# Optimization experiments

Hardware: AMD Instinct MI355X
Metric: run time of the kernel (lower is better)

## Reference

```python
import jax, jax.numpy as jnp
import numpy as np
from jax import lax

V, E, NL, NS, DC, EX = 32000, 1024, 4, 16, 4, 2
DI = EX * E          # 2048 inner dim
DTR = E // 16        # 64 dt_rank
BSZ, L = 2, 512
EPS = 1e-5


def setup_inputs() -> dict:
    key = jax.random.key(0)
    ks = jax.random.split(key, 12)
    s = 0.02
    emb = jax.random.normal(ks[0], (V, E), jnp.float32) * s
    ln_w = jnp.ones((NL, E), jnp.float32)
    ln_b = jnp.zeros((NL, E), jnp.float32)
    in_proj_w = jax.random.normal(ks[1], (NL, 2 * DI, E), jnp.float32) * s
    conv_w = jax.random.normal(ks[2], (NL, DI, DC), jnp.float32) * 0.1
    conv_b = jnp.zeros((NL, DI), jnp.float32)
    x_proj_w = jax.random.normal(ks[3], (NL, DTR + 2 * NS, DI), jnp.float32) * s
    dt_proj_w = jax.random.normal(ks[4], (NL, DI, DTR), jnp.float32) * s
    dt_proj_b = jax.random.normal(ks[5], (NL, DI), jnp.float32) * 0.1
    # canonical S4D-real init: A[d,n] = n+1  ->  A_log = log(A)
    A_log = jnp.log(jnp.tile(jnp.arange(1, NS + 1, dtype=jnp.float32)[None, None, :], (NL, DI, 1)))
    D_param = jnp.ones((NL, DI), jnp.float32)
    out_proj_w = jax.random.normal(ks[6], (NL, E, DI), jnp.float32) * s
    fln_w = jnp.ones((E,), jnp.float32)
    fln_b = jnp.zeros((E,), jnp.float32)
    input_ids = jax.random.randint(ks[7], (BSZ, L), 0, V, jnp.int64)
    targets = jax.random.randint(ks[8], (BSZ, L), 0, V, jnp.int64)
    return dict(input_ids=input_ids, targets=targets, emb=emb, ln_w=ln_w, ln_b=ln_b,
                in_proj_w=in_proj_w, conv_w=conv_w, conv_b=conv_b, x_proj_w=x_proj_w,
                dt_proj_w=dt_proj_w, dt_proj_b=dt_proj_b, A_log=A_log, D_param=D_param,
                out_proj_w=out_proj_w, fln_w=fln_w, fln_b=fln_b)


def _layer_norm(x, w, b):
    mu = x.mean(-1, keepdims=True)
    var = ((x - mu) ** 2).mean(-1, keepdims=True)
    return (x - mu) * lax.rsqrt(var + EPS) * w + b


def _mamba_block(x, in_w, cw, cb, xw, dtw, dtb, a_log, d_par, ow):
    # x: (B,L,E)
    xz = jnp.einsum('ble,fe->blf', x, in_w)          # (B,L,2*DI)
    u, res = jnp.split(xz, 2, axis=-1)               # each (B,L,DI)
    # causal depthwise conv1d, kernel width DC (left pad DC-1)
    u_pad = jnp.pad(u, ((0, 0), (DC - 1, 0), (0, 0)))
    u_conv = sum(cw[:, k] * u_pad[:, k:k + u.shape[1], :] for k in range(DC))
    u = jax.nn.silu(u_conv + cb)
    x_dbl = jnp.einsum('bld,fd->blf', u, xw)         # (B,L,DTR+2*NS)
    dt = x_dbl[..., :DTR]
    Bm = x_dbl[..., DTR:DTR + NS]                    # (B,L,NS)
    Cm = x_dbl[..., DTR + NS:]                       # (B,L,NS)
    delta = jax.nn.softplus(jnp.einsum('blr,dr->bld', dt, dtw) + dtb)  # (B,L,DI)
    A = -jnp.exp(a_log)                              # (DI,NS)
    dA = jnp.exp(delta[..., None] * A)               # (B,L,DI,NS)
    dBu = delta[..., None] * Bm[:, :, None, :] * u[..., None]

    def step(h, inp):
        dA_t, dBu_t, C_t = inp
        h = dA_t * h + dBu_t                         # (B,DI,NS)
        y = jnp.einsum('bdn,bn->bd', h, C_t)
        return h, y

    h0 = jnp.zeros((x.shape[0], DI, NS), x.dtype)
    _, ys = lax.scan(step, h0, (dA.transpose(1, 0, 2, 3), dBu.transpose(1, 0, 2, 3), Cm.transpose(1, 0, 2)))
    y = ys.transpose(1, 0, 2) + u * d_par            # (B,L,DI)
    y = y * jax.nn.silu(res)
    return jnp.einsum('bld,ed->ble', y, ow)


def reference(input_ids, targets, emb, ln_w, ln_b, in_proj_w, conv_w, conv_b,
              x_proj_w, dt_proj_w, dt_proj_b, A_log, D_param, out_proj_w, fln_w, fln_b):
    x = emb[input_ids]                               # (B,L,E)
    for l in range(NL):
        h = _layer_norm(x, ln_w[l], ln_b[l])
        h = _mamba_block(h, in_proj_w[l], conv_w[l], conv_b[l], x_proj_w[l],
                         dt_proj_w[l], dt_proj_b[l], A_log[l], D_param[l], out_proj_w[l])
        x = x + h
    x = _layer_norm(x, fln_w, fln_b)
    logits = jnp.einsum('ble,ve->blv', x, emb)       # tied lm_head
    logp = jax.nn.log_softmax(logits, axis=-1)
    valid = targets != -1
    safe_t = jnp.where(valid, targets, 0)
    nll = -jnp.take_along_axis(logp, safe_t[..., None], axis=-1)[..., 0]
    loss = jnp.where(valid, nll, 0.0).mean()
    return logits, loss
```

## Files before the change

### kernel.cpp

```cpp
#include <hip/hip_runtime.h>
#include <cstdint>
#include <cstddef>

#define L_SEQ 512
#define NBATCH 2
#define NTOK 1024
#define E_DIM 1024
#define V_DIM 32000
#define DI_DIM 2048
#define NS_DIM 16
#define DTR_DIM 64
#define DC_DIM 4
#define NL_DIM 4
#define NC 8
#define LC (L_SEQ / NC)

typedef __bf16 bf16;
typedef __bf16 bf16x8 __attribute__((ext_vector_type(8)));
typedef __bf16 bf16x4 __attribute__((ext_vector_type(4)));
typedef float  f32x4  __attribute__((ext_vector_type(4)));

__device__ __forceinline__ void gload_lds16(const void* g, void* l)
{
    __builtin_amdgcn_global_load_lds((const __attribute__((address_space(1))) uint32_t*)g,
                                     (__attribute__((address_space(3))) uint32_t*)l, 16, 0, 0);
}

__device__ __forceinline__ float softplusf(float z)
{
    return fmaxf(z, 0.0f) + log1pf(expf(-fabsf(z)));
}

__global__ void cast_f32_to_bf16(const float* __restrict__ in, bf16* __restrict__ out, int n4)
{
    int stride = gridDim.x * blockDim.x;
    for (int i = blockIdx.x * blockDim.x + threadIdx.x; i < n4; i += stride) {
        f32x4 v = ((const f32x4*)in)[i];
        bf16x4 o;
        o[0] = (bf16)v[0]; o[1] = (bf16)v[1]; o[2] = (bf16)v[2]; o[3] = (bf16)v[3];
        ((bf16x4*)out)[i] = o;
    }
}

__global__ void cast3_kernel(const float* __restrict__ a, bf16* __restrict__ oa, int na4,
                             const float* __restrict__ b, bf16* __restrict__ ob, int nb4,
                             const float* __restrict__ c, bf16* __restrict__ oc, int nc4)
{
    int stride = gridDim.x * blockDim.x;
    int tot = na4 + nb4 + nc4;
    for (int i = blockIdx.x * blockDim.x + threadIdx.x; i < tot; i += stride) {
        const float* src; bf16* dst; int k = i;
        if (k < na4) { src = a; dst = oa; }
        else if ((k -= na4) < nb4) { src = b; dst = ob; }
        else { k -= nb4; src = c; dst = oc; }
        f32x4 v = ((const f32x4*)src)[k];
        bf16x4 o;
        o[0] = (bf16)v[0]; o[1] = (bf16)v[1]; o[2] = (bf16)v[2]; o[3] = (bf16)v[3];
        ((bf16x4*)dst)[k] = o;
    }
}

__global__ void embed_kernel(const int* __restrict__ ids, const float* __restrict__ emb,
                             float* __restrict__ x)
{
    int t = blockIdx.x;
    int id = ids[t];
    ((f32x4*)(x + (size_t)t * E_DIM))[threadIdx.x] =
        ((const f32x4*)(emb + (size_t)id * E_DIM))[threadIdx.x];
}

__global__ void ln_kernel(const float* __restrict__ x, const float* __restrict__ w,
                          const float* __restrict__ b, bf16* __restrict__ out)
{
    int t = blockIdx.x;
    int tid = threadIdx.x;
    f32x4 v = ((const f32x4*)(x + (size_t)t * E_DIM))[tid];
    float s  = v[0] + v[1] + v[2] + v[3];
    float sq = v[0]*v[0] + v[1]*v[1] + v[2]*v[2] + v[3]*v[3];
#pragma unroll
    for (int off = 1; off < 64; off <<= 1) { s += __shfl_xor(s, off); sq += __shfl_xor(sq, off); }
    __shared__ float ps[4], pq[4];
    if ((tid & 63) == 0) { ps[tid >> 6] = s; pq[tid >> 6] = sq; }
    __syncthreads();
    float S  = ps[0] + ps[1] + ps[2] + ps[3];
    float SQ = pq[0] + pq[1] + pq[2] + pq[3];
    float mu  = S * (1.0f / E_DIM);
    float var = SQ * (1.0f / E_DIM) - mu * mu;
    float rs  = rsqrtf(var + 1e-5f);
    f32x4 wv = ((const f32x4*)w)[tid];
    f32x4 bv = ((const f32x4*)b)[tid];
    bf16x4 o;
#pragma unroll
    for (int i = 0; i < 4; ++i) o[i] = (bf16)((v[i] - mu) * rs * wv[i] + bv[i]);
    ((bf16x4*)(out + (size_t)t * E_DIM))[tid] = o;
}

template<int BM, int BN, int MODE, int SK>
__global__ __launch_bounds__(256) void gemm_bt(const bf16* __restrict__ A, const bf16* __restrict__ B,
                                               void* __restrict__ Cv, int K,
                                               int lda, int ldb, int ldc,
                                               const float* __restrict__ bias,
                                               int RB, int CB, int CBpad)
{
    int pid = blockIdx.x;
    int per = RB * CBpad;
    int sk  = pid / per;
    int rem = pid - sk * per;
    int xcd = rem & 7;
    int j   = rem >> 3;
    int cpx = CBpad >> 3;
    int rb  = j % RB;
    int cb  = xcd * cpx + j / RB;
    if (cb >= CB) return;
    int kseg = K / SK;
    int kbeg = sk * kseg;
    int kend = kbeg + kseg;

    __shared__ __align__(16) bf16 As[BM * 32];
    __shared__ __align__(16) bf16 Bs[BN * 32];
    int tid  = threadIdx.x;
    int lane = tid & 63;
    int wid  = tid >> 6;
    int wr = wid >> 1, wc = wid & 1;
    int li = lane & 15, lg = lane >> 4;
    const bf16* Ablk = A + (size_t)(rb * BM) * lda;
    const bf16* Bblk = B + (size_t)(cb * BN) * ldb;
    constexpr int MR  = BM / 32;
    constexpr int NR  = BN / 32;
    constexpr int TOT = (BM + BN) * 4;
    f32x4 acc[MR][NR] = {};
    for (int k0 = kbeg; k0 < kend; k0 += 32) {
        __syncthreads();
#pragma unroll
        for (int it = 0; it < TOT / 256; ++it) {
            int wbase = it * 256 + wid * 64;
            int idx   = wbase + lane;
            if (wbase < BM * 4) {
                int row = idx >> 2, seg = idx & 3;
                gload_lds16(Ablk + (size_t)row * lda + k0 + seg * 8, As + (size_t)wbase * 8);
            } else {
                int bb  = wbase - BM * 4;
                int bi  = bb + lane;
                int row = bi >> 2, seg = bi & 3;
                gload_lds16(Bblk + (size_t)row * ldb + k0 + seg * 8, Bs + (size_t)bb * 8);
            }
        }
        __syncthreads();
        bf16x8 af[MR], bfr[NR];
#pragma unroll
        for (int m = 0; m < MR; ++m) af[m]  = *(const bf16x8*)&As[(wr * (BM/2) + m * 16 + li) * 32 + lg * 8];
#pragma unroll
        for (int n = 0; n < NR; ++n) bfr[n] = *(const bf16x8*)&Bs[(wc * (BN/2) + n * 16 + li) * 32 + lg * 8];
#pragma unroll
        for (int m = 0; m < MR; ++m)
#pragma unroll
            for (int n = 0; n < NR; ++n)
                acc[m][n] = __builtin_amdgcn_mfma_f32_16x16x32_bf16(af[m], bfr[n], acc[m][n], 0, 0, 0);
    }
    int row0 = rb * BM + wr * (BM/2);
    int col0 = cb * BN + wc * (BN/2);
    float* Cf = (float*)Cv;
    bf16*  Cb = (bf16*)Cv;
#pragma unroll
    for (int m = 0; m < MR; ++m) {
#pragma unroll
        for (int n = 0; n < NR; ++n) {
            int r = row0 + m * 16 + lg * 4;
            int c = col0 + n * 16 + li;
#pragma unroll
            for (int q = 0; q < 4; ++q) {
                float v = acc[m][n][q];
                if (MODE == 0) {
                    Cf[(size_t)(r + q) * ldc + c] = v;
                } else if (MODE == 1) {
                    float* cp = Cf + (size_t)(r + q) * ldc + c;
                    *cp = v + *cp;
                } else if (MODE == 2) {
                    Cb[(size_t)(r + q) * ldc + c] = (bf16)softplusf(v + bias[c]);
                } else if (MODE == 4) {
                    Cb[(size_t)(r + q) * ldc + c] = (bf16)v;
                } else if (MODE == 5) {
                    atomicAdd(Cf + (size_t)(r + q) * ldc + c, v);
                }
            }
        }
    }
}

template<int BM, int BN, int MODE, int SK = 1>
static void launch_gemm(const bf16* A, const bf16* B, void* C, int M, int N, int K,
                        int lda, int ldb, int ldc, const float* bias, hipStream_t stream)
{
    int RB = M / BM;
    int CB = (N + BN - 1) / BN;
    int CBpad = (CB + 7) & ~7;
    gemm_bt<BM, BN, MODE, SK><<<RB * CBpad * SK, 256, 0, stream>>>(A, B, C, K, lda, ldb, ldc,
                                                                   bias, RB, CB, CBpad);
}

__global__ __launch_bounds__(256) void cxk_kernel(
        const bf16* __restrict__ xz, const float* __restrict__ cw,
        const float* __restrict__ cb, const float* __restrict__ xw,
        float* __restrict__ xdbl, bf16* __restrict__ dt_bf, bf16* __restrict__ u_bf)
{
    int t0  = blockIdx.x * 4;
    int bb  = t0 >> 9;
    int tid = threadIdx.x;
    int f   = tid & 127;
    int ks  = tid >> 7;
    __shared__ __align__(16) float sxz[7][256];
    __shared__ __align__(16) float su[4][256];
    __shared__ float pacc[4][128];
    float acc[4] = {0, 0, 0, 0};
    for (int kc = 0; kc < DI_DIM; kc += 256) {
        __syncthreads();
        if (tid < 224) {
            int row = tid >> 5, c8 = (tid & 31) * 8;
            int tr = t0 - 3 + row;
            float vals[8] = {0, 0, 0, 0, 0, 0, 0, 0};
            if (tr >= bb * L_SEQ) {
                bf16x8 v = *(const bf16x8*)&xz[(size_t)tr * (2 * DI_DIM) + kc + c8];
#pragma unroll
                for (int jj = 0; jj < 8; ++jj) vals[jj] = (float)v[jj];
            }
#pragma unroll
            for (int jj = 0; jj < 8; ++jj) sxz[row][c8 + jj] = vals[jj];
        }
        __syncthreads();
        {
            int c = tid;
            const float* cwp = cw + (size_t)(kc + c) * DC_DIM;
            float w0 = cwp[0], w1 = cwp[1], w2 = cwp[2], w3 = cwp[3];
            float bs = cb[kc + c];
#pragma unroll
            for (int tt = 0; tt < 4; ++tt) {
                float a = bs + w0 * sxz[tt][c] + w1 * sxz[tt + 1][c]
                             + w2 * sxz[tt + 2][c] + w3 * sxz[tt + 3][c];
                float uo = a / (1.0f + __expf(-a));
                su[tt][c] = uo;
                u_bf[(size_t)(t0 + tt) * DI_DIM + kc + c] = (bf16)uo;
            }
        }
        __syncthreads();
        if (f < 96) {
            int kb = ks * 128;
            for (int kk = kb; kk < kb + 128; kk += 4) {
                f32x4 wv = *(const f32x4*)&xw[(size_t)f * DI_DIM + kc + kk];
#pragma unroll
                for (int tt = 0; tt < 4; ++tt) {
                    f32x4 uv = *(f32x4*)&su[tt][kk];
                    acc[tt] += wv[0]*uv[0] + wv[1]*uv[1] + wv[2]*uv[2] + wv[3]*uv[3];
                }
            }
        }
    }
    if (ks == 1 && f < 96) {
#pragma unroll
        for (int tt = 0; tt < 4; ++tt) pacc[tt][f] = acc[tt];
    }
    __syncthreads();
    if (ks == 0 && f < 96) {
#pragma unroll
        for (int tt = 0; tt < 4; ++tt) {
            float v = acc[tt] + pacc[tt][f];
            xdbl[(size_t)(t0 + tt) * 96 + f] = v;
            if (f < 64) dt_bf[(size_t)(t0 + tt) * DTR_DIM + f] = (bf16)v;
        }
    }
}

__global__ __launch_bounds__(256) void scan_phase_a(
        const bf16* __restrict__ delta, const float* __restrict__ xdbl,
        const bf16* __restrict__ u_bf, const float* __restrict__ A_log,
        float* __restrict__ Pbuf, float* __restrict__ Sbuf)
{
    int tid = threadIdx.x;
    int c   = blockIdx.x & (NC - 1);
    int dblk= (blockIdx.x >> 3) & 127;
    int b   = blockIdx.x >> 10;
    int d0  = dblk << 4;
    int n = tid & 15, dl = tid >> 4;
    int d = d0 + dl;
    float Ac = -expf(A_log[(size_t)d * NS_DIM + n]);
    float h = 0.0f, P = 1.0f;
    __shared__ float s_dlt[32][16], s_u[32][16], s_B[32][16];
    int tt0 = tid >> 4, cc = tid & 15;
    int tbase = b * L_SEQ + c * LC;
    for (int t0 = 0; t0 < LC; t0 += 32) {
        __syncthreads();
#pragma unroll
        for (int jj = 0; jj < 2; ++jj) {
            int tt = jj * 16 + tt0;
            size_t trow = (size_t)(tbase + t0 + tt);
            s_dlt[tt][cc] = (float)delta[trow * DI_DIM + d0 + cc];
            s_u[tt][cc]   = (float)u_bf[trow * DI_DIM + d0 + cc];
            s_B[tt][cc]   = xdbl[trow * 96 + 64 + cc];
        }
        __syncthreads();
#pragma unroll
        for (int t = 0; t < 32; ++t) {
            float dlt = s_dlt[t][dl];
            float dA  = __expf(dlt * Ac);
            h = fmaf(dA, h, dlt * s_B[t][n] * s_u[t][dl]);
            P *= dA;
        }
    }
    size_t oi = (((size_t)(b * NC + c) * DI_DIM) + d) * NS_DIM + n;
    Pbuf[oi] = P;
    Sbuf[oi] = h;
}

__global__ __launch_bounds__(256) void scan_phase_c(
        const bf16* __restrict__ delta, const float* __restrict__ xdbl,
        const bf16* __restrict__ u_bf, const bf16* __restrict__ xz,
        const float* __restrict__ A_log, const float* __restrict__ D_par,
        const float* __restrict__ Pbuf, const float* __restrict__ Sbuf,
        bf16* __restrict__ y)
{
    int tid = threadIdx.x;
    int c   = blockIdx.x & (NC - 1);
    int dblk= (blockIdx.x >> 3) & 127;
    int b   = blockIdx.x >> 10;
    int d0  = dblk << 4;
    int n = tid & 15, dl = tid >> 4;
    int d = d0 + dl;
    float Ac = -expf(A_log[(size_t)d * NS_DIM + n]);
    float Dp = D_par[d];
    float h = 0.0f;
    for (int cp = 0; cp < c; ++cp) {
        size_t oi = (((size_t)(b * NC + cp) * DI_DIM) + d) * NS_DIM + n;
        h = fmaf(Pbuf[oi], h, Sbuf[oi]);
    }
    __shared__ float s_dlt[32][16], s_u[32][16], s_res[32][16], s_B[32][16], s_C[32][16];
    __shared__ bf16  s_y[32][16];
    int tt0 = tid >> 4, cc = tid & 15;
    int tbase = b * L_SEQ + c * LC;
    for (int t0 = 0; t0 < LC; t0 += 32) {
        __syncthreads();
#pragma unroll
        for (int jj = 0; jj < 2; ++jj) {
            int tt = jj * 16 + tt0;
            size_t trow = (size_t)(tbase + t0 + tt);
            s_dlt[tt][cc] = (float)delta[trow * DI_DIM + d0 + cc];
            s_u[tt][cc]   = (float)u_bf[trow * DI_DIM + d0 + cc];
            s_res[tt][cc] = (float)xz[trow * (2 * DI_DIM) + DI_DIM + d0 + cc];
            s_B[tt][cc]   = xdbl[trow * 96 + 64 + cc];
            s_C[tt][cc]   = xdbl[trow * 96 + 80 + cc];
        }
        __syncthreads();
#pragma unroll
        for (int t = 0; t < 32; ++t) {
            float dlt = s_dlt[t][dl];
            float uu  = s_u[t][dl];
            float dA  = __expf(dlt * Ac);
            float dBu = dlt * s_B[t][n] * uu;
            h = fmaf(dA, h, dBu);
            float yp = h * s_C[t][n];
            yp += __shfl_xor(yp, 1);
            yp += __shfl_xor(yp, 2);
            yp += __shfl_xor(yp, 4);
            yp += __shfl_xor(yp, 8);
            if (n == 0) {
                float res = s_res[t][dl];
                float yv  = fmaf(uu, Dp, yp) * (res / (1.0f + __expf(-res)));
                s_y[t][dl] = (bf16)yv;
            }
        }
        __syncthreads();
#pragma unroll
        for (int jj = 0; jj < 2; ++jj) {
            int tt = jj * 16 + tt0;
            size_t trow = (size_t)(tbase + t0 + tt);
            y[trow * DI_DIM + d0 + cc] = s_y[tt][cc];
        }
    }
}

__global__ void lse_nll_kernel(const float* __restrict__ logits, const int* __restrict__ targets,
                               float* __restrict__ lossp)
{
    int t = blockIdx.x, tid = threadIdx.x;
    const f32x4* row = (const f32x4*)(logits + (size_t)t * V_DIM);
    float m = -1e30f, s = 0.0f;
    for (int i = tid; i < V_DIM / 4; i += 256) {
        f32x4 v = row[i];
        float m4 = fmaxf(fmaxf(v[0], v[1]), fmaxf(v[2], v[3]));
        if (m4 > m) { s *= __expf(m - m4); m = m4; }
        s += __expf(v[0] - m) + __expf(v[1] - m) + __expf(v[2] - m) + __expf(v[3] - m);
    }
#pragma unroll
    for (int off = 1; off < 64; off <<= 1) {
        float mo = __shfl_xor(m, off), so = __shfl_xor(s, off);
        float nm = fmaxf(m, mo);
        s = s * __expf(m - nm) + so * __expf(mo - nm);
        m = nm;
    }
    __shared__ float pm[4], ps2[4];
    if ((tid & 63) == 0) { pm[tid >> 6] = m; ps2[tid >> 6] = s; }
    __syncthreads();
    if (tid == 0) {
        float M = fmaxf(fmaxf(pm[0], pm[1]), fmaxf(pm[2], pm[3]));
        float S = ps2[0] * __expf(pm[0] - M) + ps2[1] * __expf(pm[1] - M)
                + ps2[2] * __expf(pm[2] - M) + ps2[3] * __expf(pm[3] - M);
        int tg = targets[t];
        if (tg >= 0) {
            float v = (M + logf(S)) - logits[(size_t)t * V_DIM + tg];
            atomicAdd(lossp, v * (1.0f / NTOK));
        }
    }
}

extern "C" void kernel_launch(void* const* d_in, const int* in_sizes, int n_in,
                              void* d_out, int out_size, void* d_ws, size_t ws_size,
                              hipStream_t stream)
{
    const int*   ids   = (const int*)d_in[0];
    const int*   tgt   = (const int*)d_in[1];
    const float* emb   = (const float*)d_in[2];
    const float* ln_w  = (const float*)d_in[3];
    const float* ln_b  = (const float*)d_in[4];
    const float* inw   = (const float*)d_in[5];
    const float* convw = (const float*)d_in[6];
    const float* convb = (const float*)d_in[7];
    const float* xw    = (const float*)d_in[8];
    const float* dtw   = (const float*)d_in[9];
    const float* dtb   = (const float*)d_in[10];
    const float* alog  = (const float*)d_in[11];
    const float* dpar  = (const float*)d_in[12];
    const float* outw  = (const float*)d_in[13];
    const float* flnw  = (const float*)d_in[14];
    const float* flnb  = (const float*)d_in[15];
    float* logits = (float*)d_out;
    float* lossp  = logits + (size_t)NTOK * V_DIM;

    char* wsp = (char*)d_ws;
    size_t off = 0;
    auto alloc = [&](size_t bytes) -> void* {
        void* p = wsp + off;
        off += (bytes + 255) & ~(size_t)255;
        return p;
    };
    bf16*  emb_bf  = (bf16*)alloc((size_t)V_DIM * E_DIM * 2);
    bf16*  winl    = (bf16*)alloc((size_t)2 * DI_DIM * E_DIM * 2);
    bf16*  woutl   = (bf16*)alloc((size_t)E_DIM * DI_DIM * 2);
    bf16*  wdtl    = (bf16*)alloc((size_t)DI_DIM * DTR_DIM * 2);
    float* x       = (float*)alloc((size_t)NTOK * E_DIM * 4);
    bf16*  h_bf    = (bf16*)alloc((size_t)NTOK * E_DIM * 2);
    bf16*  xzb     = (bf16*)alloc((size_t)NTOK * 2 * DI_DIM * 2);
    bf16*  u_bf    = (bf16*)alloc((size_t)NTOK * DI_DIM * 2);
    float* xdbl    = (float*)alloc((size_t)NTOK * 96 * 4);
    bf16*  dt_bf   = (bf16*)alloc((size_t)NTOK * DTR_DIM * 2);
    bf16*  deltab  = (bf16*)alloc((size_t)NTOK * DI_DIM * 2);
    bf16*  y_bf    = (bf16*)alloc((size_t)NTOK * DI_DIM * 2);
    bf16*  xf_bf   = (bf16*)alloc((size_t)NTOK * E_DIM * 2);
    float* Pbuf    = (float*)alloc((size_t)NBATCH * NC * DI_DIM * NS_DIM * 4);
    float* Sbuf    = (float*)alloc((size_t)NBATCH * NC * DI_DIM * NS_DIM * 4);
    if (off > ws_size) return;

    hipMemsetAsync(lossp, 0, sizeof(float), stream);
    {
        int n4 = (int)((size_t)V_DIM * E_DIM / 4);
        cast_f32_to_bf16<<<4096, 256, 0, stream>>>(emb, emb_bf, n4);
    }
    embed_kernel<<<NTOK, 256, 0, stream>>>(ids, emb, x);

    for (int l = 0; l < NL_DIM; ++l) {
        cast3_kernel<<<2048, 256, 0, stream>>>(
            inw  + (size_t)l * 2 * DI_DIM * E_DIM, winl,  (int)((size_t)2 * DI_DIM * E_DIM / 4),
            outw + (size_t)l * E_DIM * DI_DIM,     woutl, (int)((size_t)E_DIM * DI_DIM / 4),
            dtw  + (size_t)l * DI_DIM * DTR_DIM,   wdtl,  (int)((size_t)DI_DIM * DTR_DIM / 4));

        ln_kernel<<<NTOK, 256, 0, stream>>>(x, ln_w + l * E_DIM, ln_b + l * E_DIM, h_bf);
        launch_gemm<128, 64, 4>(h_bf, winl, xzb, NTOK, 2 * DI_DIM, E_DIM,
                                E_DIM, E_DIM, 2 * DI_DIM, nullptr, stream);
        cxk_kernel<<<NTOK / 4, 256, 0, stream>>>(
            xzb, convw + (size_t)l * DI_DIM * DC_DIM, convb + (size_t)l * DI_DIM,
            xw + (size_t)l * 96 * DI_DIM, xdbl, dt_bf, u_bf);
        launch_gemm<64, 64, 2>(dt_bf, wdtl, deltab, NTOK, DI_DIM, DTR_DIM,
                               DTR_DIM, DTR_DIM, DI_DIM, dtb + (size_t)l * DI_DIM, stream);
        scan_phase_a<<<NBATCH * (DI_DIM / 16) * NC, 256, 0, stream>>>(
            deltab, xdbl, u_bf, alog + (size_t)l * DI_DIM * NS_DIM, Pbuf, Sbuf);
        scan_phase_c<<<NBATCH * (DI_DIM / 16) * NC, 256, 0, stream>>>(
            deltab, xdbl, u_bf, xzb, alog + (size_t)l * DI_DIM * NS_DIM,
            dpar + (size_t)l * DI_DIM, Pbuf, Sbuf, y_bf);
        launch_gemm<128, 128, 5, 4>(y_bf, woutl, x, NTOK, E_DIM, DI_DIM,
                                    DI_DIM, DI_DIM, E_DIM, nullptr, stream);
    }
    ln_kernel<<<NTOK, 256, 0, stream>>>(x, flnw, flnb, xf_bf);
    launch_gemm<128, 128, 0>(xf_bf, emb_bf, logits, NTOK, V_DIM, E_DIM,
                             E_DIM, E_DIM, V_DIM, nullptr, stream);
    lse_nll_kernel<<<NTOK, 256, 0, stream>>>(logits, tgt, lossp);
}
```

Baseline: 852.4 us.

## Fuse dt_proj into conv kernel, batch weight casts, and use BK=64 GEMM tiles

The dt_proj GEMM plus softplus is folded into the conv/x_proj kernel as a scalar FMA loop over dt_proj weights held in fp32, which removes one launch and the dt_bf round trip. Weight casts for all layers now run in one kernel up front when the workspace is large enough, replacing four per-layer casts. The GEMM template gains a BK parameter and all GEMMs now use K tiles of 64, halving barrier count per K step at the cost of more LDS. The fused dt loop reads 2048x64 fp32 weights per block, which could add redundant global traffic.

```diff
diff --git a/kernel.cpp b/kernel.cpp
--- a/kernel.cpp
+++ b/kernel.cpp
@@ -42,17 +42,15 @@
     }
 }
 
-__global__ void cast3_kernel(const float* __restrict__ a, bf16* __restrict__ oa, int na4,
-                             const float* __restrict__ b, bf16* __restrict__ ob, int nb4,
-                             const float* __restrict__ c, bf16* __restrict__ oc, int nc4)
+__global__ void cast2_kernel(const float* __restrict__ a, bf16* __restrict__ oa, int na4,
+                             const float* __restrict__ b, bf16* __restrict__ ob, int nb4)
 {
     int stride = gridDim.x * blockDim.x;
-    int tot = na4 + nb4 + nc4;
+    int tot = na4 + nb4;
     for (int i = blockIdx.x * blockDim.x + threadIdx.x; i < tot; i += stride) {
         const float* src; bf16* dst; int k = i;
         if (k < na4) { src = a; dst = oa; }
-        else if ((k -= na4) < nb4) { src = b; dst = ob; }
-        else { k -= nb4; src = c; dst = oc; }
+        else { k -= na4; src = b; dst = ob; }
         f32x4 v = ((const f32x4*)src)[k];
         bf16x4 o;
         o[0] = (bf16)v[0]; o[1] = (bf16)v[1]; o[2] = (bf16)v[2]; o[3] = (bf16)v[3];
@@ -95,11 +93,10 @@
     ((bf16x4*)(out + (size_t)t * E_DIM))[tid] = o;
 }
 
-template<int BM, int BN, int MODE, int SK>
+template<int BM, int BN, int BK, int MODE, int SK>
 __global__ __launch_bounds__(256) void gemm_bt(const bf16* __restrict__ A, const bf16* __restrict__ B,
                                                void* __restrict__ Cv, int K,
                                                int lda, int ldb, int ldc,
-                                               const float* __restrict__ bias,
                                                int RB, int CB, int CBpad)
 {
     int pid = blockIdx.x;
@@ -116,8 +113,8 @@
     int kbeg = sk * kseg;
     int kend = kbeg + kseg;
 
-    __shared__ __align__(16) bf16 As[BM * 32];
-    __shared__ __align__(16) bf16 Bs[BN * 32];
+    __shared__ __align__(16) bf16 As[BM * BK];
+    __shared__ __align__(16) bf16 Bs[BN * BK];
     int tid  = threadIdx.x;
     int lane = tid & 63;
     int wid  = tid >> 6;
@@ -125,37 +122,44 @@
     int li = lane & 15, lg = lane >> 4;
     const bf16* Ablk = A + (size_t)(rb * BM) * lda;
     const bf16* Bblk = B + (size_t)(cb * BN) * ldb;
-    constexpr int MR  = BM / 32;
-    constexpr int NR  = BN / 32;
-    constexpr int TOT = (BM + BN) * 4;
+    constexpr int MR   = BM / 32;
+    constexpr int NR   = BN / 32;
+    constexpr int SEGS = BK / 8;
+    constexpr int AOPS = BM * SEGS;
+    constexpr int TOT  = (BM + BN) * SEGS;
     f32x4 acc[MR][NR] = {};
-    for (int k0 = kbeg; k0 < kend; k0 += 32) {
+    for (int k0 = kbeg; k0 < kend; k0 += BK) {
         __syncthreads();
 #pragma unroll
         for (int it = 0; it < TOT / 256; ++it) {
             int wbase = it * 256 + wid * 64;
             int idx   = wbase + lane;
-            if (wbase < BM * 4) {
-                int row = idx >> 2, seg = idx & 3;
+            if (wbase < AOPS) {
+                int row = idx / SEGS, seg = idx % SEGS;
                 gload_lds16(Ablk + (size_t)row * lda + k0 + seg * 8, As + (size_t)wbase * 8);
             } else {
-                int bb  = wbase - BM * 4;
+                int bb  = wbase - AOPS;
                 int bi  = bb + lane;
-                int row = bi >> 2, seg = bi & 3;
+                int row = bi / SEGS, seg = bi % SEGS;
                 gload_lds16(Bblk + (size_t)row * ldb + k0 + seg * 8, Bs + (size_t)bb * 8);
             }
         }
         __syncthreads();
-        bf16x8 af[MR], bfr[NR];
-#pragma unroll
-        for (int m = 0; m < MR; ++m) af[m]  = *(const bf16x8*)&As[(wr * (BM/2) + m * 16 + li) * 32 + lg * 8];
-#pragma unroll
-        for (int n = 0; n < NR; ++n) bfr[n] = *(const bf16x8*)&Bs[(wc * (BN/2) + n * 16 + li) * 32 + lg * 8];
-#pragma unroll
-        for (int m = 0; m < MR; ++m)
+#pragma unroll
+        for (int kk = 0; kk < BK / 32; ++kk) {
+            bf16x8 af[MR], bfr[NR];
+#pragma unroll
+            for (int m = 0; m < MR; ++m)
+                af[m]  = *(const bf16x8*)&As[(wr * (BM/2) + m * 16 + li) * BK + kk * 32 + lg * 8];
 #pragma unroll
             for (int n = 0; n < NR; ++n)
-                acc[m][n] = __builtin_amdgcn_mfma_f32_16x16x32_bf16(af[m], bfr[n], acc[m][n], 0, 0, 0);
+                bfr[n] = *(const bf16x8*)&Bs[(wc * (BN/2) + n * 16 + li) * BK + kk * 32 + lg * 8];
+#pragma unroll
+            for (int m = 0; m < MR; ++m)
+#pragma unroll
+                for (int n = 0; n < NR; ++n)
+                    acc[m][n] = __builtin_amdgcn_mfma_f32_16x16x32_bf16(af[m], bfr[n], acc[m][n], 0, 0, 0);
+        }
     }
     int row0 = rb * BM + wr * (BM/2);
     int col0 = cb * BN + wc * (BN/2);
@@ -172,11 +176,6 @@
                 float v = acc[m][n][q];
                 if (MODE == 0) {
                     Cf[(size_t)(r + q) * ldc + c] = v;
-                } else if (MODE == 1) {
-                    float* cp = Cf + (size_t)(r + q) * ldc + c;
-                    *cp = v + *cp;
-                } else if (MODE == 2) {
-                    Cb[(size_t)(r + q) * ldc + c] = (bf16)softplusf(v + bias[c]);
                 } else if (MODE == 4) {
                     Cb[(size_t)(r + q) * ldc + c] = (bf16)v;
                 } else if (MODE == 5) {
@@ -187,21 +186,22 @@
     }
 }
 
-template<int BM, int BN, int MODE, int SK = 1>
+template<int BM, int BN, int BK, int MODE, int SK = 1>
 static void launch_gemm(const bf16* A, const bf16* B, void* C, int M, int N, int K,
-                        int lda, int ldb, int ldc, const float* bias, hipStream_t stream)
+                        int lda, int ldb, int ldc, hipStream_t stream)
 {
     int RB = M / BM;
     int CB = (N + BN - 1) / BN;
     int CBpad = (CB + 7) & ~7;
-    gemm_bt<BM, BN, MODE, SK><<<RB * CBpad * SK, 256, 0, stream>>>(A, B, C, K, lda, ldb, ldc,
-                                                                   bias, RB, CB, CBpad);
+    gemm_bt<BM, BN, BK, MODE, SK><<<RB * CBpad * SK, 256, 0, stream>>>(A, B, C, K, lda, ldb, ldc,
+                                                                       RB, CB, CBpad);
 }
 
 __global__ __launch_bounds__(256) void cxk_kernel(
         const bf16* __restrict__ xz, const float* __restrict__ cw,
         const float* __restrict__ cb, const float* __restrict__ xw,
-        float* __restrict__ xdbl, bf16* __restrict__ dt_bf, bf16* __restrict__ u_bf)
+        const float* __restrict__ dtw, const float* __restrict__ dtb,
+        float* __restrict__ xdbl, bf16* __restrict__ delta, bf16* __restrict__ u_bf)
 {
     int t0  = blockIdx.x * 4;
     int bb  = t0 >> 9;
@@ -211,6 +211,7 @@
     __shared__ __align__(16) float sxz[7][256];
     __shared__ __align__(16) float su[4][256];
     __shared__ float pacc[4][128];
+    __shared__ float s_dt[4][64];
     float acc[4] = {0, 0, 0, 0};
     for (int kc = 0; kc < DI_DIM; kc += 256) {
         __syncthreads();
@@ -264,8 +265,32 @@
         for (int tt = 0; tt < 4; ++tt) {
             float v = acc[tt] + pacc[tt][f];
             xdbl[(size_t)(t0 + tt) * 96 + f] = v;
-            if (f < 64) dt_bf[(size_t)(t0 + tt) * DTR_DIM + f] = (bf16)v;
-        }
+            if (f < 64) s_dt[tt][f] = v;
+        }
+    }
+    __syncthreads();
+#pragma unroll
+    for (int i = 0; i < DI_DIM / 256; ++i) {
+        int d = i * 256 + tid;
+        const float* wrow = dtw + (size_t)d * DTR_DIM;
+        float bs = dtb[d];
+        float a0 = bs, a1 = bs, a2 = bs, a3 = bs;
+#pragma unroll
+        for (int k = 0; k < DTR_DIM; k += 4) {
+            f32x4 wv = *(const f32x4*)&wrow[k];
+#pragma unroll
+            for (int kk = 0; kk < 4; ++kk) {
+                float w = wv[kk];
+                a0 = fmaf(w, s_dt[0][k + kk], a0);
+                a1 = fmaf(w, s_dt[1][k + kk], a1);
+                a2 = fmaf(w, s_dt[2][k + kk], a2);
+                a3 = fmaf(w, s_dt[3][k + kk], a3);
+            }
+        }
+        delta[(size_t)(t0 + 0) * DI_DIM + d] = (bf16)softplusf(a0);
+        delta[(size_t)(t0 + 1) * DI_DIM + d] = (bf16)softplusf(a1);
+        delta[(size_t)(t0 + 2) * DI_DIM + d] = (bf16)softplusf(a2);
+        delta[(size_t)(t0 + 3) * DI_DIM + d] = (bf16)softplusf(a3);
     }
 }
 
@@ -433,6 +458,9 @@
     float* logits = (float*)d_out;
     float* lossp  = logits + (size_t)NTOK * V_DIM;
 
+    const size_t INW_L  = (size_t)2 * DI_DIM * E_DIM;
+    const size_t OUTW_L = (size_t)E_DIM * DI_DIM;
+
     char* wsp = (char*)d_ws;
     size_t off = 0;
     auto alloc = [&](size_t bytes) -> void* {
@@ -441,20 +469,28 @@
         return p;
     };
     bf16*  emb_bf  = (bf16*)alloc((size_t)V_DIM * E_DIM * 2);
-    bf16*  winl    = (bf16*)alloc((size_t)2 * DI_DIM * E_DIM * 2);
-    bf16*  woutl   = (bf16*)alloc((size_t)E_DIM * DI_DIM * 2);
-    bf16*  wdtl    = (bf16*)alloc((size_t)DI_DIM * DTR_DIM * 2);
     float* x       = (float*)alloc((size_t)NTOK * E_DIM * 4);
     bf16*  h_bf    = (bf16*)alloc((size_t)NTOK * E_DIM * 2);
     bf16*  xzb     = (bf16*)alloc((size_t)NTOK * 2 * DI_DIM * 2);
     bf16*  u_bf    = (bf16*)alloc((size_t)NTOK * DI_DIM * 2);
     float* xdbl    = (float*)alloc((size_t)NTOK * 96 * 4);
-    bf16*  dt_bf   = (bf16*)alloc((size_t)NTOK * DTR_DIM * 2);
     bf16*  deltab  = (bf16*)alloc((size_t)NTOK * DI_DIM * 2);
     bf16*  y_bf    = (bf16*)alloc((size_t)NTOK * DI_DIM * 2);
     bf16*  xf_bf   = (bf16*)alloc((size_t)NTOK * E_DIM * 2);
     float* Pbuf    = (float*)alloc((size_t)NBATCH * NC * DI_DIM * NS_DIM * 4);
     float* Sbuf    = (float*)alloc((size_t)NBATCH * NC * DI_DIM * NS_DIM * 4);
+    size_t base = off;
+    size_t big_need = base + (((size_t)NL_DIM * INW_L * 2 + 255) & ~(size_t)255)
+                           + (((size_t)NL_DIM * OUTW_L * 2 + 255) & ~(size_t)255);
+    bool big = (big_need <= ws_size);
+    bf16* winl; bf16* woutl;
+    if (big) {
+        winl  = (bf16*)alloc((size_t)NL_DIM * INW_L * 2);
+        woutl = (bf16*)alloc((size_t)NL_DIM * OUTW_L * 2);
+    } else {
+        winl  = (bf16*)alloc(INW_L * 2);
+        woutl = (bf16*)alloc(OUTW_L * 2);
+    }
     if (off > ws_size) return;
 
     hipMemsetAsync(lossp, 0, sizeof(float), stream);
@@ -462,32 +498,39 @@
         int n4 = (int)((size_t)V_DIM * E_DIM / 4);
         cast_f32_to_bf16<<<4096, 256, 0, stream>>>(emb, emb_bf, n4);
     }
+    if (big) {
+        cast2_kernel<<<4096, 256, 0, stream>>>(
+            inw,  winl,  (int)((size_t)NL_DIM * INW_L / 4),
+            outw, woutl, (int)((size_t)NL_DIM * OUTW_L / 4));
+    }
     embed_kernel<<<NTOK, 256, 0, stream>>>(ids, emb, x);
 
     for (int l = 0; l < NL_DIM; ++l) {
-        cast3_kernel<<<2048, 256, 0, stream>>>(
-            inw  + (size_t)l * 2 * DI_DIM * E_DIM, winl,  (int)((size_t)2 * DI_DIM * E_DIM / 4),
-            outw + (size_t)l * E_DIM * DI_DIM,     woutl, (int)((size_t)E_DIM * DI_DIM / 4),
-            dtw  + (size_t)l * DI_DIM * DTR_DIM,   wdtl,  (int)((size_t)DI_DIM * DTR_DIM / 4));
-
+        const bf16* wi = big ? winl  + (size_t)l * INW_L  : winl;
+        const bf16* wo = big ? woutl + (size_t)l * OUTW_L : woutl;
+        if (!big) {
+            cast2_kernel<<<2048, 256, 0, stream>>>(
+                inw  + (size_t)l * INW_L,  winl,  (int)(INW_L / 4),
+                outw + (size_t)l * OUTW_L, woutl, (int)(OUTW_L / 4));
+        }
         ln_kernel<<<NTOK, 256, 0, stream>>>(x, ln_w + l * E_DIM, ln_b + l * E_DIM, h_bf);
-        launch_gemm<128, 64, 4>(h_bf, winl, xzb, NTOK, 2 * DI_DIM, E_DIM,
-                                E_DIM, E_DIM, 2 * DI_DIM, nullptr, stream);
+        launch_gemm<128, 64, 64, 4>(h_bf, wi, xzb, NTOK, 2 * DI_DIM, E_DIM,
+                                    E_DIM, E_DIM, 2 * DI_DIM, stream);
         cxk_kernel<<<NTOK / 4, 256, 0, stream>>>(
             xzb, convw + (size_t)l * DI_DIM * DC_DIM, convb + (size_t)l * DI_DIM,
-            xw + (size_t)l * 96 * DI_DIM, xdbl, dt_bf, u_bf);
-        launch_gemm<64, 64, 2>(dt_bf, wdtl, deltab, NTOK, DI_DIM, DTR_DIM,
-                               DTR_DIM, DTR_DIM, DI_DIM, dtb + (size_t)l * DI_DIM, stream);
+            xw + (size_t)l * 96 * DI_DIM,
+            dtw + (size_t)l * DI_DIM * DTR_DIM, dtb + (size_t)l * DI_DIM,
+            xdbl, deltab, u_bf);
         scan_phase_a<<<NBATCH * (DI_DIM / 16) * NC, 256, 0, stream>>>(
             deltab, xdbl, u_bf, alog + (size_t)l * DI_DIM * NS_DIM, Pbuf, Sbuf);
         scan_phase_c<<<NBATCH * (DI_DIM / 16) * NC, 256, 0, stream>>>(
             deltab, xdbl, u_bf, xzb, alog + (size_t)l * DI_DIM * NS_DIM,
             dpar + (size_t)l * DI_DIM, Pbuf, Sbuf, y_bf);
-        launch_gemm<128, 128, 5, 4>(y_bf, woutl, x, NTOK, E_DIM, DI_DIM,
-                                    DI_DIM, DI_DIM, E_DIM, nullptr, stream);
+        launch_gemm<128, 128, 64, 5, 4>(y_bf, wo, x, NTOK, E_DIM, DI_DIM,
+                                        DI_DIM, DI_DIM, E_DIM, stream);
     }
     ln_kernel<<<NTOK, 256, 0, stream>>>(x, flnw, flnb, xf_bf);
-    launch_gemm<128, 128, 0>(xf_bf, emb_bf, logits, NTOK, V_DIM, E_DIM,
-                             E_DIM, E_DIM, V_DIM, nullptr, stream);
+    launch_gemm<128, 128, 64, 0>(xf_bf, emb_bf, logits, NTOK, V_DIM, E_DIM,
+                                 E_DIM, E_DIM, V_DIM, stream);
     lse_nll_kernel<<<NTOK, 256, 0, stream>>>(logits, tgt, lossp);
 }
```

After: 1.167 ms. +36.9%, slower.
